# Optimization experiments

Hardware: AMD Instinct MI355X
Metric: run time of the kernel (lower is better)

The kernel has to match this reference:

```python
import jax, jax.numpy as jnp
import numpy as np

B, DIM, S = 8, 512, 1024
H, DH = 8, 64
FF_INNER = 1024      # dim * (ff_mult//2)
CONV_INNER = 1024    # dim * expansion_factor
K = 31
PAD = (K - 1) // 2


def _bn(x, g, b):
    # eval-mode BatchNorm2d with running stats (0,1) absorbed: per-channel affine
    return x * g[None, :, None, None] + b[None, :, None, None]


def _pw(x, w, b):
    # 1x1 Conv2d == channel matmul. x: [B,C,S,1], w: [O,C]
    return jnp.einsum('oc,bcst->bost', w, x) + b[None, :, None, None]


def _ff(x, g, b, w1, b1, w2, b2):
    h = _pw(_bn(x, g, b), w1, b1)
    return _pw(jax.nn.silu(h), w2, b2)


def _attn(x, g, b, wq, bq, wk, bk, wv, bv, wo, bo):
    xn = _bn(x, g, b)
    q = _pw(xn, wq, bq)[..., 0].reshape(B, H, DH, S)
    k = _pw(xn, wk, bk)[..., 0].reshape(B, H, DH, S)
    v = _pw(xn, wv, bv)[..., 0].reshape(B, H, DH, S)
    scale = DH ** -0.5
    scores = jnp.einsum('bhds,bhdt->bhst', q, k) * scale   # [B,H,S,S]
    w = jax.nn.softmax(scores, axis=-1)
    o = jnp.einsum('bhst,bhdt->bhds', w, v).reshape(B, H * DH, S)[..., None]
    return _pw(o, wo, bo)


def _conv(x, g, b, pw1_w, pw1_b, dconv_w, dconv_b, cbn_g, cbn_b, pw2_w, pw2_b):
    h = _pw(_bn(x, g, b), pw1_w, pw1_b)          # [B,2*CONV_INNER,S,1]
    a, gate = jnp.split(h, 2, axis=1)
    h = a * jax.nn.sigmoid(gate)                  # GLU
    h = jnp.transpose(h, (0, 1, 3, 2))            # [B,C,1,S] so kernel (1,K) runs along seq
    h = jax.lax.conv_general_dilated(
        h, dconv_w, window_strides=(1, 1), padding=((0, 0), (PAD, PAD)),
        dimension_numbers=('NCHW', 'OIHW', 'NCHW'))
    h = jnp.transpose(h, (0, 1, 3, 2)) + dconv_b[None, :, None, None]
    h = jax.nn.silu(_bn(h, cbn_g, cbn_b))
    return _pw(h, pw2_w, pw2_b)


def setup_inputs() -> dict:
    key = jax.random.key(0)
    ks = iter(jax.random.split(key, 32))
    w = lambda *s: jax.random.normal(next(ks), s, jnp.float32) * 0.02
    d = {
        'x': jax.random.normal(next(ks), (B, DIM, S, 1), jnp.float32),
        'ff1_g': jnp.ones((DIM,)), 'ff1_b': jnp.zeros((DIM,)),
        'ff1_w1': w(FF_INNER, DIM), 'ff1_b1': jnp.zeros((FF_INNER,)),
        'ff1_w2': w(DIM, FF_INNER), 'ff1_b2': jnp.zeros((DIM,)),
        'attn_g': jnp.ones((DIM,)), 'attn_b': jnp.zeros((DIM,)),
        'wq': w(H * DH, DIM), 'bq': jnp.zeros((H * DH,)),
        'wk': w(H * DH, DIM), 'bk': jnp.zeros((H * DH,)),
        'wv': w(H * DH, DIM), 'bv': jnp.zeros((H * DH,)),
        'wo': w(DIM, H * DH), 'bo': jnp.zeros((DIM,)),
        'conv_g': jnp.ones((DIM,)), 'conv_b': jnp.zeros((DIM,)),
        'pw1_w': w(2 * CONV_INNER, DIM), 'pw1_b': jnp.zeros((2 * CONV_INNER,)),
        'dconv_w': w(CONV_INNER, CONV_INNER, 1, K), 'dconv_b': jnp.zeros((CONV_INNER,)),
        'cbn_g': jnp.ones((CONV_INNER,)), 'cbn_b': jnp.zeros((CONV_INNER,)),
        'pw2_w': w(DIM, CONV_INNER), 'pw2_b': jnp.zeros((DIM,)),
        'ff2_g': jnp.ones((DIM,)), 'ff2_b': jnp.zeros((DIM,)),
        'ff2_w1': w(FF_INNER, DIM), 'ff2_b1': jnp.zeros((FF_INNER,)),
        'ff2_w2': w(DIM, FF_INNER), 'ff2_b2': jnp.zeros((DIM,)),
        'fin_g': jnp.ones((DIM,)), 'fin_b': jnp.zeros((DIM,)),
    }
    return d


def reference(x, ff1_g, ff1_b, ff1_w1, ff1_b1, ff1_w2, ff1_b2,
              attn_g, attn_b, wq, bq, wk, bk, wv, bv, wo, bo,
              conv_g, conv_b, pw1_w, pw1_b, dconv_w, dconv_b, cbn_g, cbn_b, pw2_w, pw2_b,
              ff2_g, ff2_b, ff2_w1, ff2_b1, ff2_w2, ff2_b2, fin_g, fin_b):
    x1 = x + 0.5 * _ff(x, ff1_g, ff1_b, ff1_w1, ff1_b1, ff1_w2, ff1_b2)
    x2 = x1 + _attn(x1, attn_g, attn_b, wq, bq, wk, bk, wv, bv, wo, bo)
    x3 = x2 + _conv(x2, conv_g, conv_b, pw1_w, pw1_b, dconv_w, dconv_b, cbn_g, cbn_b, pw2_w, pw2_b)
    x4 = x3 + 0.5 * _ff(x3, ff2_g, ff2_b, ff2_w1, ff2_b1, ff2_w2, ff2_b2)
    return _bn(x4, fin_g, fin_b)
```

## Files before the change

kernel.cpp:

```cpp
#include <hip/hip_runtime.h>
#include <cstdint>
#include <cstddef>

using bf16 = __bf16;
typedef __bf16 bf16x8 __attribute__((ext_vector_type(8)));
typedef float f32x4 __attribute__((ext_vector_type(4)));
typedef unsigned int uint4v __attribute__((ext_vector_type(4)));

#define NB 8
#define DIM 512
#define SEQ 1024
#define NH 8
#define DH 64
#define CONV_INNER 1024
#define KW 31
#define PADW 15
#define HPRA 1056

__device__ __forceinline__ float fsigmoid(float x) { return 1.f / (1.f + __expf(-x)); }
__device__ __forceinline__ float fsilu(float x) { return x * fsigmoid(x); }

__device__ __forceinline__ void gld16(const bf16* g, bf16* l) {
  __builtin_amdgcn_global_load_lds(
      (const __attribute__((address_space(1))) unsigned int*)g,
      (__attribute__((address_space(3))) unsigned int*)l, 16, 0, 0);
}


__global__ __launch_bounds__(256) void k_diag(float* __restrict__ out, int n, float v) {
  int i = blockIdx.x * 256 + threadIdx.x;
  if (i < n) out[i] = v;
}


__global__ __launch_bounds__(256) void k_convert_bf16(const float* __restrict__ src,
                                                      bf16* __restrict__ dst, int n) {
  int i = (blockIdx.x * 256 + threadIdx.x) * 4;
  if (i + 3 < n) {
    float4 v = *reinterpret_cast<const float4*>(src + i);
    dst[i]     = (bf16)v.x;
    dst[i + 1] = (bf16)v.y;
    dst[i + 2] = (bf16)v.z;
    dst[i + 3] = (bf16)v.w;
  }
}

__global__ __launch_bounds__(256) void k_conv_wt(const float* __restrict__ w,
                                                 bf16* __restrict__ wt) {
  __shared__ float t[256 * KW];
  int o = blockIdx.x, i0 = blockIdx.y * 256;
  const float* src = w + (size_t)o * (CONV_INNER * KW) + (size_t)i0 * KW;
  for (int idx = threadIdx.x; idx < 256 * KW; idx += 256) t[idx] = src[idx];
  __syncthreads();
  for (int k = 0; k < KW; ++k) {
    wt[((size_t)k * CONV_INNER + o) * CONV_INNER + i0 + threadIdx.x] =
        (bf16)t[threadIdx.x * KW + k];
  }
}

__global__ __launch_bounds__(256) void k_pad_zero(bf16* __restrict__ hpad) {
  int i = blockIdx.x * 256 + threadIdx.x;
  int b = i / (32 * 128);
  int r = (i >> 7) & 31;
  int c8 = (i & 127) * 8;
  int row = (r < PADW) ? r : 1024 + r;
  uint4v z = {0u, 0u, 0u, 0u};
  *reinterpret_cast<uint4v*>(&hpad[((size_t)b * HPRA + row) * CONV_INNER + c8]) = z;
}

__global__ __launch_bounds__(256) void k_transpose_in(const float* __restrict__ x,
                                                      const float* __restrict__ g,
                                                      const float* __restrict__ bvec,
                                                      float* __restrict__ xT,
                                                      bf16* __restrict__ xbn) {
  __shared__ float t[32][33];
  int s0 = blockIdx.x * 32, c0 = blockIdx.y * 32, b = blockIdx.z;
  int col = threadIdx.x & 31, rq = threadIdx.x >> 5;
#pragma unroll
  for (int i = 0; i < 4; ++i) {
    int row = rq + i * 8;
    t[row][col] = x[((size_t)b * DIM + c0 + row) * SEQ + s0 + col];
  }
  __syncthreads();
  float gg = g[c0 + col], bb = bvec[c0 + col];
#pragma unroll
  for (int i = 0; i < 4; ++i) {
    int srow = rq + i * 8;
    float v = t[col][srow];
    size_t off = ((size_t)b * SEQ + s0 + srow) * DIM + c0 + col;
    xT[off] = v;
    xbn[off] = (bf16)(v * gg + bb);
  }
}

__global__ __launch_bounds__(256) void k_concat_bias(const float* __restrict__ bq,
                                                     const float* __restrict__ bk,
                                                     const float* __restrict__ bv,
                                                     float* __restrict__ qb) {
  int i = blockIdx.x * 256 + threadIdx.x;
  if (i < 512) qb[i] = bq[i];
  else if (i < 1024) qb[i] = bk[i - 512];
  else if (i < 1536) qb[i] = bv[i - 1024];
}

template <int EPI>
__global__ __launch_bounds__(256) void k_gemm(const bf16* __restrict__ A,
                                              const bf16* __restrict__ W,
                                              const float* __restrict__ bias,
                                              const float* __restrict__ res,
                                              const float* __restrict__ g,
                                              const float* __restrict__ bb,
                                              float* __restrict__ outf,
                                              bf16* __restrict__ outb, int N, int K) {
  __shared__ __align__(16) bf16 sA[2][128 * 64];
  __shared__ __align__(16) bf16 sB[2][128 * 64];
  const int tid = threadIdx.x;
  const int b = blockIdx.z;
  const int m0 = blockIdx.y * 128, n0 = blockIdx.x * 128;
  const int lane = tid & 63, wid = tid >> 6;
  const int wm = (wid & 1) * 64, wn = (wid >> 1) * 64;
  const int fr = lane & 15, fg = lane >> 4;
  const int srow = lane >> 3;
  const int scol = ((lane & 7) ^ srow) * 8;

  f32x4 acc[4][4];
#pragma unroll
  for (int i = 0; i < 4; ++i)
#pragma unroll
    for (int j = 0; j < 4; ++j) acc[i][j] = (f32x4)0.f;

  const bf16* Abase = A + ((size_t)b * SEQ + m0 + srow) * K + scol;
  const bf16* Wbase = W + (size_t)(n0 + srow) * K + scol;
  const int nch = K >> 6;

#pragma unroll
  for (int c = 0; c < 4; ++c) {
    const int ch = wid + c * 4;
    gld16(Abase + (size_t)(ch * 8) * K, &sA[0][ch * 512]);
    gld16(Wbase + (size_t)(ch * 8) * K, &sB[0][ch * 512]);
  }
  __syncthreads();

  int buf = 0;
  for (int kt = 0; kt < nch; ++kt) {
    if (kt + 1 < nch) {
      const int kc = (kt + 1) * 64;
#pragma unroll
      for (int c = 0; c < 4; ++c) {
        const int ch = wid + c * 4;
        gld16(Abase + (size_t)(ch * 8) * K + kc, &sA[buf ^ 1][ch * 512]);
        gld16(Wbase + (size_t)(ch * 8) * K + kc, &sB[buf ^ 1][ch * 512]);
      }
    }
#pragma unroll
    for (int kk = 0; kk < 2; ++kk) {
      const int cg = kk * 4 + fg;
      bf16x8 aF[4], bF[4];
#pragma unroll
      for (int i = 0; i < 4; ++i) {
        const int ar = wm + i * 16 + fr;
        aF[i] = *reinterpret_cast<const bf16x8*>(
            &sA[buf][ar * 64 + ((cg ^ (ar & 7)) * 8)]);
        const int br = wn + i * 16 + fr;
        bF[i] = *reinterpret_cast<const bf16x8*>(
            &sB[buf][br * 64 + ((cg ^ (br & 7)) * 8)]);
      }
#pragma unroll
      for (int mi = 0; mi < 4; ++mi)
#pragma unroll
        for (int ni = 0; ni < 4; ++ni)
          acc[mi][ni] = __builtin_amdgcn_mfma_f32_16x16x32_bf16(aF[mi], bF[ni],
                                                                acc[mi][ni], 0, 0, 0);
    }
    __syncthreads();
    buf ^= 1;
  }

#pragma unroll
  for (int mi = 0; mi < 4; ++mi) {
#pragma unroll
    for (int ni = 0; ni < 4; ++ni) {
      int ncol = n0 + wn + ni * 16 + fr;
      float bv = bias[ncol];
      if constexpr (EPI == 5) {
        float gg = g[ncol], bbv = bb[ncol];
        int mrow0 = m0 + wm + mi * 16 + fg * 4;
        float v[4];
#pragma unroll
        for (int j = 0; j < 4; ++j) {
          float a = acc[mi][ni][j] + bv;
          float r = res[((size_t)b * SEQ + mrow0 + j) * 512 + ncol] + 0.5f * a;
          v[j] = r * gg + bbv;
        }
        *reinterpret_cast<float4*>(outf + ((size_t)b * 512 + ncol) * SEQ + mrow0) =
            make_float4(v[0], v[1], v[2], v[3]);
      } else {
#pragma unroll
        for (int j = 0; j < 4; ++j) {
          int mrow = m0 + wm + mi * 16 + fg * 4 + j;
          size_t off = ((size_t)b * SEQ + mrow) * N + ncol;
          float a = acc[mi][ni][j] + bv;
          if constexpr (EPI == 0) {
            outb[off] = (bf16)fsilu(a);
          } else if constexpr (EPI == 2) {
            outb[off] = (bf16)a;
          } else if constexpr (EPI == 1) {
            float r = res[off] + 0.5f * a;
            outf[off] = r;
            outb[off] = (bf16)(r * g[ncol] + bb[ncol]);
          } else if constexpr (EPI == 3) {
            float r = res[off] + a;
            outf[off] = r;
            outb[off] = (bf16)(r * g[ncol] + bb[ncol]);
          }
        }
      }
    }
  }
}

__global__ __launch_bounds__(256) void k_pw1_glu(const bf16* __restrict__ A,
                                                 const bf16* __restrict__ W,
                                                 const float* __restrict__ bias,
                                                 bf16* __restrict__ hpad) {
  __shared__ __align__(16) bf16 sA[128 * 64];
  __shared__ __align__(16) bf16 sBa[128 * 64];
  __shared__ __align__(16) bf16 sBg[128 * 64];
  const int tid = threadIdx.x;
  const int b = blockIdx.z;
  const int m0 = blockIdx.y * 128, n0 = blockIdx.x * 128;
  const int lane = tid & 63, wid = tid >> 6;
  const int wm = (wid & 1) * 64, wn = (wid >> 1) * 64;
  const int fr = lane & 15, fg = lane >> 4;
  const int srow = lane >> 3;
  const int scol = ((lane & 7) ^ srow) * 8;
  const int K = 512;

  f32x4 accA[4][4], accG[4][4];
#pragma unroll
  for (int i = 0; i < 4; ++i)
#pragma unroll
    for (int j = 0; j < 4; ++j) { accA[i][j] = (f32x4)0.f; accG[i][j] = (f32x4)0.f; }

  const bf16* Abase = A + ((size_t)b * SEQ + m0 + srow) * K + scol;
  const bf16* WaB = W + (size_t)(n0 + srow) * K + scol;
  const bf16* WgB = W + (size_t)(n0 + 1024 + srow) * K + scol;

  for (int kt = 0; kt < 8; ++kt) {
    const int kc = kt * 64;
#pragma unroll
    for (int c = 0; c < 4; ++c) {
      const int ch = wid + c * 4;
      gld16(Abase + (size_t)(ch * 8) * K + kc, &sA[ch * 512]);
      gld16(WaB + (size_t)(ch * 8) * K + kc, &sBa[ch * 512]);
      gld16(WgB + (size_t)(ch * 8) * K + kc, &sBg[ch * 512]);
    }
    __syncthreads();
#pragma unroll
    for (int kk = 0; kk < 2; ++kk) {
      const int cg = kk * 4 + fg;
      bf16x8 aF[4], bFa[4], bFg[4];
#pragma unroll
      for (int i = 0; i < 4; ++i) {
        const int ar = wm + i * 16 + fr;
        aF[i] = *reinterpret_cast<const bf16x8*>(
            &sA[ar * 64 + ((cg ^ (ar & 7)) * 8)]);
        const int br = wn + i * 16 + fr;
        bFa[i] = *reinterpret_cast<const bf16x8*>(
            &sBa[br * 64 + ((cg ^ (br & 7)) * 8)]);
        bFg[i] = *reinterpret_cast<const bf16x8*>(
            &sBg[br * 64 + ((cg ^ (br & 7)) * 8)]);
      }
#pragma unroll
      for (int mi = 0; mi < 4; ++mi)
#pragma unroll
        for (int ni = 0; ni < 4; ++ni) {
          accA[mi][ni] =
              __builtin_amdgcn_mfma_f32_16x16x32_bf16(aF[mi], bFa[ni], accA[mi][ni], 0, 0, 0);
          accG[mi][ni] =
              __builtin_amdgcn_mfma_f32_16x16x32_bf16(aF[mi], bFg[ni], accG[mi][ni], 0, 0, 0);
        }
    }
    __syncthreads();
  }

#pragma unroll
  for (int mi = 0; mi < 4; ++mi) {
#pragma unroll
    for (int ni = 0; ni < 4; ++ni) {
      int ncol = n0 + wn + ni * 16 + fr;
      float ba = bias[ncol], bg = bias[ncol + 1024];
#pragma unroll
      for (int j = 0; j < 4; ++j) {
        int mrow = m0 + wm + mi * 16 + fg * 4 + j;
        float av = accA[mi][ni][j] + ba;
        float gv = accG[mi][ni][j] + bg;
        hpad[((size_t)b * HPRA + PADW + mrow) * CONV_INNER + ncol] =
            (bf16)(av * fsigmoid(gv));
      }
    }
  }
}

__global__ __launch_bounds__(256) void k_conv(const bf16* __restrict__ hpad,
                                              const bf16* __restrict__ wt,
                                              const float* __restrict__ bias,
                                              const float* __restrict__ g,
                                              const float* __restrict__ bb,
                                              bf16* __restrict__ outb) {
  __shared__ __align__(16) bf16 sA[160 * 64];
  __shared__ __align__(16) bf16 sBb[3][128 * 64];
  const int tid = threadIdx.x;
  const int b = blockIdx.z;
  const int n0 = blockIdx.x * 128, m0 = blockIdx.y * 128;
  const int lane = tid & 63, wid = tid >> 6;
  const int wm = (wid & 1) * 64, wn = (wid >> 1) * 64;
  const int fr = lane & 15, fg = lane >> 4;
  const int srow = lane >> 3;
  const int scol = ((lane & 7) ^ srow) * 8;
  const size_t WKS = (size_t)CONV_INNER * CONV_INNER;

  f32x4 acc[4][4];
#pragma unroll
  for (int i = 0; i < 4; ++i)
#pragma unroll
    for (int j = 0; j < 4; ++j) acc[i][j] = (f32x4)0.f;

  const bf16* Abase = hpad + ((size_t)b * HPRA + m0 + srow) * CONV_INNER + scol;
  const bf16* Wbase = wt + (size_t)(n0 + srow) * CONV_INNER + scol;

  for (int it = 0; it < 16; ++it) {
    const int itc = it * 64;
#pragma unroll
    for (int c = 0; c < 5; ++c) {
      const int ch = wid + c * 4;
      gld16(Abase + (size_t)(ch * 8) * CONV_INNER + itc, &sA[ch * 512]);
    }
#pragma unroll
    for (int c = 0; c < 4; ++c) {
      const int ch = wid + c * 4;
      gld16(Wbase + (size_t)(ch * 8) * CONV_INNER + itc, &sBb[0][ch * 512]);
    }
#pragma unroll
    for (int c = 0; c < 4; ++c) {
      const int ch = wid + c * 4;
      gld16(Wbase + WKS + (size_t)(ch * 8) * CONV_INNER + itc, &sBb[1][ch * 512]);
    }
    asm volatile("s_waitcnt vmcnt(4)" ::: "memory");
    __builtin_amdgcn_s_barrier();

    const bf16* bcur = sBb[0];
    const bf16* bnext = sBb[1];
    bf16* bfill = sBb[2];
    for (int ks = 0; ks < KW; ++ks) {
      if (ks + 2 < KW) {
#pragma unroll
        for (int c = 0; c < 4; ++c) {
          const int ch = wid + c * 4;
          gld16(Wbase + (size_t)(ks + 2) * WKS + (size_t)(ch * 8) * CONV_INNER + itc,
                bfill + ch * 512);
        }
      }
#pragma unroll
      for (int kk = 0; kk < 2; ++kk) {
        const int cg = kk * 4 + fg;
        bf16x8 aF[4], bF[4];
#pragma unroll
        for (int i = 0; i < 4; ++i) {
          const int ar = ks + wm + i * 16 + fr;
          aF[i] = *reinterpret_cast<const bf16x8*>(
              &sA[ar * 64 + ((cg ^ (ar & 7)) * 8)]);
        }
#pragma unroll
        for (int n = 0; n < 4; ++n) {
          const int br = wn + n * 16 + fr;
          bF[n] = *reinterpret_cast<const bf16x8*>(
              &bcur[br * 64 + ((cg ^ (br & 7)) * 8)]);
        }
#pragma unroll
        for (int mi = 0; mi < 4; ++mi)
#pragma unroll
          for (int ni = 0; ni < 4; ++ni)
            acc[mi][ni] = __builtin_amdgcn_mfma_f32_16x16x32_bf16(aF[mi], bF[ni],
                                                                  acc[mi][ni], 0, 0, 0);
      }
      if (ks + 2 < KW) {
        asm volatile("s_waitcnt vmcnt(4)" ::: "memory");
      } else {
        asm volatile("s_waitcnt vmcnt(0)" ::: "memory");
      }
      __builtin_amdgcn_s_barrier();
      const bf16* t = bcur;
      bcur = bnext;
      bnext = bfill;
      bfill = (bf16*)t;
    }
  }

#pragma unroll
  for (int mi = 0; mi < 4; ++mi) {
#pragma unroll
    for (int ni = 0; ni < 4; ++ni) {
      int ncol = n0 + wn + ni * 16 + fr;
      float bv = bias[ncol], gg = g[ncol], bbv = bb[ncol];
#pragma unroll
      for (int j = 0; j < 4; ++j) {
        int mrow = m0 + wm + mi * 16 + fg * 4 + j;
        float a = acc[mi][ni][j] + bv;
        outb[((size_t)b * SEQ + mrow) * CONV_INNER + ncol] = (bf16)fsilu(a * gg + bbv);
      }
    }
  }
}

__global__ __launch_bounds__(256) void k_attn(const bf16* __restrict__ qkv,
                                              bf16* __restrict__ out) {
  __shared__ __align__(16) bf16 sQ[128][72];
  __shared__ __align__(16) bf16 sK[64][72];
  __shared__ __align__(16) bf16 sVT[64][72];
  __shared__ __align__(16) bf16 sP[128][72];
  const int tid = threadIdx.x;
  const int bh = blockIdx.y;
  const int b = bh >> 3, h = bh & 7;
  const int m0 = blockIdx.x * 128;
  const int lane = tid & 63, wid = tid >> 6;
  const int w32 = wid * 32;
  const int fr = lane & 15, fg = lane >> 4;
  const size_t base = (size_t)b * SEQ * 1536;

  for (int idx = tid; idx < 128 * 8; idx += 256) {
    int row = idx >> 3, c = (idx & 7) * 8;
    *reinterpret_cast<uint4v*>(&sQ[row][c]) =
        *reinterpret_cast<const uint4v*>(qkv + base + (size_t)(m0 + row) * 1536 + h * 64 + c);
  }

  f32x4 o[2][4];
  float mst[2][4], lst[2][4];
#pragma unroll
  for (int mi = 0; mi < 2; ++mi)
#pragma unroll
    for (int j = 0; j < 4; ++j) {
      mst[mi][j] = -1e30f;
      lst[mi][j] = 0.f;
#pragma unroll
      for (int df = 0; df < 4; ++df) o[mi][df] = (f32x4)0.f;
    }

  for (int t0 = 0; t0 < SEQ; t0 += 64) {
    for (int idx = tid; idx < 64 * 8; idx += 256) {
      int row = idx >> 3, c = (idx & 7) * 8;
      *reinterpret_cast<uint4v*>(&sK[row][c]) = *reinterpret_cast<const uint4v*>(
          qkv + base + (size_t)(t0 + row) * 1536 + 512 + h * 64 + c);
    }
    for (int e = tid; e < 64 * 64; e += 256) {
      int t = e >> 6, d = e & 63;
      sVT[d][t] = qkv[base + (size_t)(t0 + t) * 1536 + 1024 + h * 64 + d];
    }
    __syncthreads();

    f32x4 sacc[2][4];
#pragma unroll
    for (int mi = 0; mi < 2; ++mi)
#pragma unroll
      for (int tf = 0; tf < 4; ++tf) sacc[mi][tf] = (f32x4)0.f;
#pragma unroll
    for (int kk = 0; kk < 2; ++kk) {
      bf16x8 aQ[2], bK[4];
#pragma unroll
      for (int mi = 0; mi < 2; ++mi)
        aQ[mi] = *reinterpret_cast<const bf16x8*>(&sQ[w32 + mi * 16 + fr][kk * 32 + fg * 8]);
#pragma unroll
      for (int tf = 0; tf < 4; ++tf)
        bK[tf] = *reinterpret_cast<const bf16x8*>(&sK[tf * 16 + fr][kk * 32 + fg * 8]);
#pragma unroll
      for (int mi = 0; mi < 2; ++mi)
#pragma unroll
        for (int tf = 0; tf < 4; ++tf)
          sacc[mi][tf] =
              __builtin_amdgcn_mfma_f32_16x16x32_bf16(aQ[mi], bK[tf], sacc[mi][tf], 0, 0, 0);
    }

#pragma unroll
    for (int mi = 0; mi < 2; ++mi) {
#pragma unroll
      for (int j = 0; j < 4; ++j) {
        float rm = -1e30f;
#pragma unroll
        for (int tf = 0; tf < 4; ++tf) rm = fmaxf(rm, sacc[mi][tf][j] * 0.125f);
#pragma unroll
        for (int off = 1; off < 16; off <<= 1) rm = fmaxf(rm, __shfl_xor(rm, off));
        float mnew = fmaxf(mst[mi][j], rm);
        float al = __expf(mst[mi][j] - mnew);
        float ps = 0.f;
#pragma unroll
        for (int tf = 0; tf < 4; ++tf) {
          float p = __expf(sacc[mi][tf][j] * 0.125f - mnew);
          ps += p;
          sP[w32 + mi * 16 + fg * 4 + j][tf * 16 + fr] = (bf16)p;
        }
#pragma unroll
        for (int off = 1; off < 16; off <<= 1) ps += __shfl_xor(ps, off);
        lst[mi][j] = lst[mi][j] * al + ps;
        mst[mi][j] = mnew;
#pragma unroll
        for (int df = 0; df < 4; ++df) o[mi][df][j] *= al;
      }
    }
    __syncthreads();

#pragma unroll
    for (int kk = 0; kk < 2; ++kk) {
      bf16x8 aP[2], bV[4];
#pragma unroll
      for (int mi = 0; mi < 2; ++mi)
        aP[mi] = *reinterpret_cast<const bf16x8*>(&sP[w32 + mi * 16 + fr][kk * 32 + fg * 8]);
#pragma unroll
      for (int df = 0; df < 4; ++df)
        bV[df] = *reinterpret_cast<const bf16x8*>(&sVT[df * 16 + fr][kk * 32 + fg * 8]);
#pragma unroll
      for (int mi = 0; mi < 2; ++mi)
#pragma unroll
        for (int df = 0; df < 4; ++df)
          o[mi][df] = __builtin_amdgcn_mfma_f32_16x16x32_bf16(aP[mi], bV[df], o[mi][df], 0, 0, 0);
    }
    __syncthreads();
  }

#pragma unroll
  for (int mi = 0; mi < 2; ++mi)
#pragma unroll
    for (int df = 0; df < 4; ++df)
#pragma unroll
      for (int j = 0; j < 4; ++j) {
        int row = m0 + w32 + mi * 16 + fg * 4 + j;
        int col = h * 64 + df * 16 + fr;
        out[((size_t)b * SEQ + row) * 512 + col] = (bf16)(o[mi][df][j] / lst[mi][j]);
      }
}


extern "C" void kernel_launch(void* const* d_in, const int* in_sizes, int n_in,
                              void* d_out, int out_size, void* d_ws, size_t ws_size,
                              hipStream_t stream) {
  const float* x      = (const float*)d_in[0];
  const float* ff1_g  = (const float*)d_in[1];
  const float* ff1_b  = (const float*)d_in[2];
  const float* ff1_w1 = (const float*)d_in[3];
  const float* ff1_b1 = (const float*)d_in[4];
  const float* ff1_w2 = (const float*)d_in[5];
  const float* ff1_b2 = (const float*)d_in[6];
  const float* attn_g = (const float*)d_in[7];
  const float* attn_b = (const float*)d_in[8];
  const float* wq     = (const float*)d_in[9];
  const float* bq     = (const float*)d_in[10];
  const float* wk     = (const float*)d_in[11];
  const float* bk     = (const float*)d_in[12];
  const float* wv     = (const float*)d_in[13];
  const float* bv     = (const float*)d_in[14];
  const float* wo     = (const float*)d_in[15];
  const float* bo     = (const float*)d_in[16];
  const float* conv_g = (const float*)d_in[17];
  const float* conv_b = (const float*)d_in[18];
  const float* pw1_w  = (const float*)d_in[19];
  const float* pw1_b  = (const float*)d_in[20];
  const float* dconv_w = (const float*)d_in[21];
  const float* dconv_b = (const float*)d_in[22];
  const float* cbn_g  = (const float*)d_in[23];
  const float* cbn_b  = (const float*)d_in[24];
  const float* pw2_w  = (const float*)d_in[25];
  const float* pw2_b  = (const float*)d_in[26];
  const float* ff2_g  = (const float*)d_in[27];
  const float* ff2_b  = (const float*)d_in[28];
  const float* ff2_w1 = (const float*)d_in[29];
  const float* ff2_b1 = (const float*)d_in[30];
  const float* ff2_w2 = (const float*)d_in[31];
  const float* ff2_b2 = (const float*)d_in[32];
  const float* fin_g  = (const float*)d_in[33];
  const float* fin_b  = (const float*)d_in[34];

  char* ws = (char*)d_ws;
  size_t off = 0;
  auto alloc = [&](size_t bytes) -> void* {
    off = (off + 255) & ~(size_t)255;
    void* p = ws + off;
    off += bytes;
    return p;
  };

  bf16* wqkv  = (bf16*)alloc((size_t)1536 * 512 * 2);
  float* qkvb = (float*)alloc(1536 * 4);
  bf16* wf1a  = (bf16*)alloc((size_t)1024 * 512 * 2);
  bf16* wf1b  = (bf16*)alloc((size_t)512 * 1024 * 2);
  bf16* wwo   = (bf16*)alloc((size_t)512 * 512 * 2);
  bf16* wpw1  = (bf16*)alloc((size_t)2048 * 512 * 2);
  bf16* wpw2  = (bf16*)alloc((size_t)512 * 1024 * 2);
  bf16* wf2a  = (bf16*)alloc((size_t)1024 * 512 * 2);
  bf16* wf2b  = (bf16*)alloc((size_t)512 * 1024 * 2);

  bf16*  Bn  = (bf16*)alloc((size_t)NB * SEQ * 512 * 2);
  float* F1  = (float*)alloc((size_t)NB * SEQ * 512 * 4);
  bf16*  HGp = (bf16*)alloc((size_t)NB * HPRA * 1024 * 2);
  bf16*  H2  = (bf16*)alloc((size_t)NB * SEQ * 1024 * 2);

  char* E = (char*)alloc((size_t)KW * 1024 * 1024 * 2);
  bf16*  wt     = (bf16*)E;
  bf16*  h1     = (bf16*)E;
  bf16*  qkv    = (bf16*)E;
  bf16*  attn_o = (bf16*)(E + (size_t)24 * 1024 * 1024);
  float* x1     = (float*)(E + (size_t)32 * 1024 * 1024);
  float* x3     = (float*)E;
  bf16*  h3     = (bf16*)(E + (size_t)16 * 1024 * 1024);

  float* xT = F1;
  float* x2 = F1;
  bf16* xbn = Bn, *x1bn = Bn, *x2bn = Bn, *x3bn = Bn;
  size_t needed = off;
  (void)in_sizes; (void)n_in;

  if (ws_size < needed) {
    k_diag<<<(out_size + 255) / 256, 256, 0, stream>>>(
        (float*)d_out, out_size, (float)(ws_size >> 20));
    return;
  }

  auto cvt = [&](const float* s, bf16* d, int n) {
    k_convert_bf16<<<n / 1024, 256, 0, stream>>>(s, d, n);
  };
  cvt(wq, wqkv, 512 * 512);
  cvt(wk, wqkv + 512 * 512, 512 * 512);
  cvt(wv, wqkv + 1024 * 512, 512 * 512);
  cvt(ff1_w1, wf1a, 1024 * 512);
  cvt(ff1_w2, wf1b, 512 * 1024);
  cvt(wo, wwo, 512 * 512);
  cvt(pw1_w, wpw1, 2048 * 512);
  cvt(pw2_w, wpw2, 512 * 1024);
  cvt(ff2_w1, wf2a, 1024 * 512);
  cvt(ff2_w2, wf2b, 512 * 1024);
  k_concat_bias<<<6, 256, 0, stream>>>(bq, bk, bv, qkvb);
  k_pad_zero<<<(NB * 32 * 128) / 256, 256, 0, stream>>>(HGp);
  k_transpose_in<<<dim3(32, 16, NB), 256, 0, stream>>>(x, ff1_g, ff1_b, xT, xbn);

  k_gemm<0><<<dim3(8, 8, NB), 256, 0, stream>>>(xbn, wf1a, ff1_b1, nullptr, nullptr,
                                                nullptr, nullptr, h1, 1024, 512);
  k_gemm<1><<<dim3(4, 8, NB), 256, 0, stream>>>(h1, wf1b, ff1_b2, xT, attn_g, attn_b,
                                                x1, x1bn, 512, 1024);
  k_gemm<2><<<dim3(12, 8, NB), 256, 0, stream>>>(x1bn, wqkv, qkvb, nullptr, nullptr,
                                                 nullptr, nullptr, qkv, 1536, 512);
  k_attn<<<dim3(8, 64), 256, 0, stream>>>(qkv, attn_o);
  k_gemm<3><<<dim3(4, 8, NB), 256, 0, stream>>>(attn_o, wwo, bo, x1, conv_g, conv_b,
                                                x2, x2bn, 512, 512);
  k_conv_wt<<<dim3(1024, 4), 256, 0, stream>>>(dconv_w, wt);
  k_pw1_glu<<<dim3(8, 8, NB), 256, 0, stream>>>(x2bn, wpw1, pw1_b, HGp);
  k_conv<<<dim3(8, 8, NB), 256, 0, stream>>>(HGp, wt, dconv_b, cbn_g, cbn_b, H2);
  k_gemm<3><<<dim3(4, 8, NB), 256, 0, stream>>>(H2, wpw2, pw2_b, x2, ff2_g, ff2_b,
                                                x3, x3bn, 512, 1024);
  k_gemm<0><<<dim3(8, 8, NB), 256, 0, stream>>>(x3bn, wf2a, ff2_b1, nullptr, nullptr,
                                                nullptr, nullptr, h3, 1024, 512);
  k_gemm<5><<<dim3(4, 8, NB), 256, 0, stream>>>(h3, wf2b, ff2_b2, x3, fin_g, fin_b,
                                                (float*)d_out, nullptr, 512, 1024);
}
```

Measured before the change: 802.4 us.

## Batch weight conversions into one launch and double-buffer depthwise conv weights

Merges the ten per-weight fp32-to-bf16 conversion launches into one kernel that finds each block's segment from a cumulative block table, removing launch overhead. In the conv kernel it also replaces the three-slot weight pipeline (prefetch two taps ahead, partial vmcnt waits) with a two-slot buffer that prefetches one tap ahead and uses full __syncthreads. This lowers LDS use, which may help occupancy, but exposes more global-load latency on each of the 31 tap steps.

```diff
diff --git a/kernel.cpp b/kernel.cpp
--- a/kernel.cpp
+++ b/kernel.cpp
@@ -33,16 +33,26 @@
 }
 
 
-__global__ __launch_bounds__(256) void k_convert_bf16(const float* __restrict__ src,
-                                                      bf16* __restrict__ dst, int n) {
-  int i = (blockIdx.x * 256 + threadIdx.x) * 4;
-  if (i + 3 < n) {
-    float4 v = *reinterpret_cast<const float4*>(src + i);
-    dst[i]     = (bf16)v.x;
-    dst[i + 1] = (bf16)v.y;
-    dst[i + 2] = (bf16)v.z;
-    dst[i + 3] = (bf16)v.w;
-  }
+struct CvtArgs {
+  const float* s[10];
+  bf16* d[10];
+  int cum[11];
+};
+
+__global__ __launch_bounds__(256) void k_convert_all(CvtArgs a) {
+  int blk = blockIdx.x;
+  int seg = 0;
+#pragma unroll
+  for (int t = 0; t < 10; ++t)
+    if (blk >= a.cum[t + 1]) seg = t + 1;
+  const float* src = a.s[seg];
+  bf16* dst = a.d[seg];
+  int i = ((blk - a.cum[seg]) * 256 + threadIdx.x) * 4;
+  float4 v = *reinterpret_cast<const float4*>(src + i);
+  dst[i]     = (bf16)v.x;
+  dst[i + 1] = (bf16)v.y;
+  dst[i + 2] = (bf16)v.z;
+  dst[i + 3] = (bf16)v.w;
 }
 
 __global__ __launch_bounds__(256) void k_conv_wt(const float* __restrict__ w,
@@ -309,7 +319,8 @@
                                               const float* __restrict__ bb,
                                               bf16* __restrict__ outb) {
   __shared__ __align__(16) bf16 sA[160 * 64];
-  __shared__ __align__(16) bf16 sBb[3][128 * 64];
+  __shared__ __align__(16) bf16 sB0[128 * 64];
+  __shared__ __align__(16) bf16 sB1[128 * 64];
   const int tid = threadIdx.x;
   const int b = blockIdx.z;
   const int n0 = blockIdx.x * 128, m0 = blockIdx.y * 128;
@@ -318,7 +329,6 @@
   const int fr = lane & 15, fg = lane >> 4;
   const int srow = lane >> 3;
   const int scol = ((lane & 7) ^ srow) * 8;
-  const size_t WKS = (size_t)CONV_INNER * CONV_INNER;
 
   f32x4 acc[4][4];
 #pragma unroll
@@ -339,26 +349,20 @@
 #pragma unroll
     for (int c = 0; c < 4; ++c) {
       const int ch = wid + c * 4;
-      gld16(Wbase + (size_t)(ch * 8) * CONV_INNER + itc, &sBb[0][ch * 512]);
-    }
-#pragma unroll
-    for (int c = 0; c < 4; ++c) {
-      const int ch = wid + c * 4;
-      gld16(Wbase + WKS + (size_t)(ch * 8) * CONV_INNER + itc, &sBb[1][ch * 512]);
-    }
-    asm volatile("s_waitcnt vmcnt(4)" ::: "memory");
-    __builtin_amdgcn_s_barrier();
-
-    const bf16* bcur = sBb[0];
-    const bf16* bnext = sBb[1];
-    bf16* bfill = sBb[2];
+      gld16(Wbase + (size_t)(ch * 8) * CONV_INNER + itc, &sB0[ch * 512]);
+    }
+    __syncthreads();
+
     for (int ks = 0; ks < KW; ++ks) {
-      if (ks + 2 < KW) {
+      const bf16* cur = (ks & 1) ? sB1 : sB0;
+      bf16* nxt = (ks & 1) ? sB0 : sB1;
+      if (ks + 1 < KW) {
 #pragma unroll
         for (int c = 0; c < 4; ++c) {
           const int ch = wid + c * 4;
-          gld16(Wbase + (size_t)(ks + 2) * WKS + (size_t)(ch * 8) * CONV_INNER + itc,
-                bfill + ch * 512);
+          gld16(Wbase + (size_t)(ks + 1) * CONV_INNER * CONV_INNER +
+                    (size_t)(ch * 8) * CONV_INNER + itc,
+                &nxt[ch * 512]);
         }
       }
 #pragma unroll
@@ -375,7 +379,7 @@
         for (int n = 0; n < 4; ++n) {
           const int br = wn + n * 16 + fr;
           bF[n] = *reinterpret_cast<const bf16x8*>(
-              &bcur[br * 64 + ((cg ^ (br & 7)) * 8)]);
+              &cur[br * 64 + ((cg ^ (br & 7)) * 8)]);
         }
 #pragma unroll
         for (int mi = 0; mi < 4; ++mi)
@@ -384,16 +388,7 @@
             acc[mi][ni] = __builtin_amdgcn_mfma_f32_16x16x32_bf16(aF[mi], bF[ni],
                                                                   acc[mi][ni], 0, 0, 0);
       }
-      if (ks + 2 < KW) {
-        asm volatile("s_waitcnt vmcnt(4)" ::: "memory");
-      } else {
-        asm volatile("s_waitcnt vmcnt(0)" ::: "memory");
-      }
-      __builtin_amdgcn_s_barrier();
-      const bf16* t = bcur;
-      bcur = bnext;
-      bnext = bfill;
-      bfill = (bf16*)t;
+      __syncthreads();
     }
   }
 
@@ -623,19 +618,22 @@
     return;
   }
 
-  auto cvt = [&](const float* s, bf16* d, int n) {
-    k_convert_bf16<<<n / 1024, 256, 0, stream>>>(s, d, n);
-  };
-  cvt(wq, wqkv, 512 * 512);
-  cvt(wk, wqkv + 512 * 512, 512 * 512);
-  cvt(wv, wqkv + 1024 * 512, 512 * 512);
-  cvt(ff1_w1, wf1a, 1024 * 512);
-  cvt(ff1_w2, wf1b, 512 * 1024);
-  cvt(wo, wwo, 512 * 512);
-  cvt(pw1_w, wpw1, 2048 * 512);
-  cvt(pw2_w, wpw2, 512 * 1024);
-  cvt(ff2_w1, wf2a, 1024 * 512);
-  cvt(ff2_w2, wf2b, 512 * 1024);
+  CvtArgs ca;
+  ca.s[0] = wq;      ca.d[0] = wqkv;
+  ca.s[1] = wk;      ca.d[1] = wqkv + 512 * 512;
+  ca.s[2] = wv;      ca.d[2] = wqkv + 1024 * 512;
+  ca.s[3] = ff1_w1;  ca.d[3] = wf1a;
+  ca.s[4] = ff1_w2;  ca.d[4] = wf1b;
+  ca.s[5] = wo;      ca.d[5] = wwo;
+  ca.s[6] = pw1_w;   ca.d[6] = wpw1;
+  ca.s[7] = pw2_w;   ca.d[7] = wpw2;
+  ca.s[8] = ff2_w1;  ca.d[8] = wf2a;
+  ca.s[9] = ff2_w2;  ca.d[9] = wf2b;
+  int blocks1024[10] = {256, 256, 256, 512, 512, 256, 1024, 512, 512, 512};
+  int cum = 0;
+  for (int i = 0; i < 10; ++i) { ca.cum[i] = cum; cum += blocks1024[i]; }
+  ca.cum[10] = cum;
+  k_convert_all<<<cum, 256, 0, stream>>>(ca);
   k_concat_bias<<<6, 256, 0, stream>>>(bq, bk, bv, qkvb);
   k_pad_zero<<<(NB * 32 * 128) / 256, 256, 0, stream>>>(HGp);
   k_transpose_in<<<dim3(32, 16, NB), 256, 0, stream>>>(x, ff1_g, ff1_b, xT, xbn);
```

Measured after the change: 761.7 us. 1.05x faster.
